# Performance work log

Measured on AMD Instinct MI355X. Metric: run time of the kernel, lower is better.

The kernel has to match this reference:

```python
import jax, jax.numpy as jnp
import numpy as np

SEQ_LEN = 12
EMB = 64        # embedding_dim
H = 128         # dec_h_dim
MLP = 1024      # mlp_dim
Z = 32          # z_dim
ZX = MLP + Z    # 1056, width of cat([enc_h_feat, z])
B = 32768


def setup_inputs() -> dict:
    key = jax.random.key(0)
    ks = jax.random.split(key, 16)
    s = 0.05  # weight scale to keep the recurrence stable
    return {
        "last_pos": jax.random.normal(ks[0], (B, 2), jnp.float32),
        "last_pos_rel": jax.random.normal(ks[1], (B, 2), jnp.float32),
        "enc_h_feat": jax.random.normal(ks[2], (B, MLP), jnp.float32),
        "z": jax.random.normal(ks[3], (B, Z), jnp.float32),
        "seq_start_end": jnp.zeros((1, 2), jnp.int64),
        # LSTM params (PyTorch layout: gates ordered i,f,g,o along rows)
        "W_ih": jax.random.normal(ks[4], (4 * H, ZX + EMB), jnp.float32) * s,
        "W_hh": jax.random.normal(ks[5], (4 * H, H), jnp.float32) * s,
        "b_ih": jax.random.normal(ks[6], (4 * H,), jnp.float32) * s,
        "b_hh": jax.random.normal(ks[7], (4 * H,), jnp.float32) * s,
        # mlp: Linear(ZX->MLP), ReLU, Linear(MLP->H), ReLU
        "W1": jax.random.normal(ks[8], (MLP, ZX), jnp.float32) * s,
        "b1": jax.random.normal(ks[9], (MLP,), jnp.float32) * s,
        "W2": jax.random.normal(ks[10], (H, MLP), jnp.float32) * s,
        "b2": jax.random.normal(ks[11], (H,), jnp.float32) * s,
        # spatial_embedding: Linear(2 -> EMB)
        "W_sp": jax.random.normal(ks[12], (EMB, 2), jnp.float32) * s,
        "b_sp": jax.random.normal(ks[13], (EMB,), jnp.float32) * s,
        # hidden2pos: Linear(H -> 2)
        "W_hp": jax.random.normal(ks[14], (2, H), jnp.float32) * s,
        "b_hp": jax.random.normal(ks[15], (2,), jnp.float32) * s,
    }


def _decode(last_pos, last_pos_rel, enc_h_feat, z,
            W_ih, W_hh, b_ih, b_hh, W1, b1, W2, b2, W_sp, b_sp, W_hp, b_hp):
    # initial decoder input from last relative position
    dec_inp = last_pos_rel @ W_sp.T + b_sp                     # [B, EMB]
    zx = jnp.concatenate([enc_h_feat, z], axis=1)              # [B, ZX]
    h = jax.nn.relu(jax.nn.relu(zx @ W1.T + b1) @ W2.T + b2)   # [B, H]
    c = jnp.zeros_like(h)
    # zx is constant across steps: precompute its gate contribution + biases
    W_zx, W_emb = W_ih[:, :ZX], W_ih[:, ZX:]
    zx_proj = zx @ W_zx.T + b_ih + b_hh                        # [B, 4H]

    def step(carry, _):
        h, c, last_pos, dec_inp = carry
        gates = zx_proj + dec_inp @ W_emb.T + h @ W_hh.T       # [B, 4H]
        i, f, g, o = jnp.split(gates, 4, axis=1)
        c = jax.nn.sigmoid(f) * c + jax.nn.sigmoid(i) * jnp.tanh(g)
        h = jax.nn.sigmoid(o) * jnp.tanh(c)
        rel_pos = h @ W_hp.T + b_hp                            # [B, 2]
        last_pos = rel_pos + last_pos
        dec_inp = rel_pos @ W_sp.T + b_sp
        return (h, c, last_pos, dec_inp), rel_pos

    _, pred = jax.lax.scan(step, (h, c, last_pos, dec_inp), None, length=SEQ_LEN)
    return pred  # [SEQ_LEN, B, 2]


def reference(last_pos, last_pos_rel, enc_h_feat, z, seq_start_end,
              W_ih, W_hh, b_ih, b_hh, W1, b1, W2, b2, W_sp, b_sp, W_hp, b_hp):
    # seq_start_end is unused by the original forward
    return _decode(last_pos, last_pos_rel, enc_h_feat, z,
                   W_ih, W_hh, b_ih, b_hh, W1, b1, W2, b2, W_sp, b_sp, W_hp, b_hp)
```

## Files before the change

### kernel.cpp

```cpp
#include <hip/hip_runtime.h>

#define BATCH   32768
#define SEQLEN  12
#define EMB     64
#define H       128
#define MLP     1024
#define Z       32
#define ZX      1056
#define KP      1088
#define NG      512

typedef _Float16 f16x8 __attribute__((ext_vector_type(8)));
typedef float    f32x4 __attribute__((ext_vector_type(4)));

#define S_WCAT_OFF   0u
#define S_W2H_OFF    3244032u
#define S_WHHF_OFF   3506176u
#define S_WC_OFF     3637248u
#define S_BIAS2_OFF  3641344u
#define S_T1_OFF     3643392u
#define S_GP_OFF     70752256u
#define S_H0_OFF     137861120u
#define B_WCAT_OFF   0u
#define B_W2H_OFF    3342336u
#define B_WHHF_OFF   3604480u
#define B_WC_OFF     3735552u
#define B_BIAS2_OFF  3739648u
#define B_T1_OFF     3741696u
#define B_GP_OFF     70850560u
#define B_H0_OFF     137959424u
#define B_ZX16_OFF   146348032u
#define B_TOTAL      217651200ull

__device__ __forceinline__ float sigf(float x) {
    return __builtin_amdgcn_rcpf(1.0f + __expf(-x));
}
__device__ __forceinline__ float tanhfast(float x) {
    return 2.0f * __builtin_amdgcn_rcpf(1.0f + __expf(-2.0f * x)) - 1.0f;
}

__device__ __forceinline__ void gload16(const void* g, void* l) {
    __builtin_amdgcn_global_load_lds(
        (const __attribute__((address_space(1))) unsigned int*)(unsigned long long)(uintptr_t)g,
        (__attribute__((address_space(3))) unsigned int*)(unsigned int)(uintptr_t)l,
        16, 0, 0);
}

__global__ __launch_bounds__(256) void prep_kernel(
    const float* __restrict__ W_ih, const float* __restrict__ W_hh_in,
    const float* __restrict__ b_ih, const float* __restrict__ b_hh,
    const float* __restrict__ W1,   const float* __restrict__ W2,
    const float* __restrict__ W_sp, const float* __restrict__ b_sp,
    const float* __restrict__ W_hp, int cs,
    _Float16* __restrict__ wcat, _Float16* __restrict__ w2h,
    _Float16* __restrict__ whhf, float* __restrict__ wc, float* __restrict__ bias2)
{
    const int bid = blockIdx.x;
    const int tid = threadIdx.x;
    if (bid < 1536) {
        const float* src = (bid < 1024) ? (W1 + (size_t)bid * ZX)
                                        : (W_ih + (size_t)(bid - 1024) * 1120);
        _Float16* dst = wcat + (size_t)bid * cs;
        for (int k = tid; k < cs; k += 256)
            dst[k] = (k < ZX) ? (_Float16)src[k] : (_Float16)0.f;
    } else if (bid < 1664) {
        const int n = bid - 1536;
        for (int k = tid; k < MLP; k += 256)
            w2h[n * MLP + k] = (_Float16)W2[n * MLP + k];
    } else if (bid < 1920) {
        const int n = (bid - 1664) * 2 + (tid >> 7);
        const int k = tid & 127;
        float wc0 = 0.f, wc1 = 0.f;
        for (int e = 0; e < EMB; ++e) {
            const float we = W_ih[(size_t)n * 1120 + ZX + e];
            wc0 += we * W_sp[e * 2];
            wc1 += we * W_sp[e * 2 + 1];
        }
        whhf[n * H + k] = (_Float16)(W_hh_in[n * H + k] + wc0 * W_hp[k] + wc1 * W_hp[H + k]);
    } else {
        const int t = (bid - 1920) * 256 + tid;
        if (t < 1024) {
            const int n = t >> 1, j = t & 1;
            float s = 0.f;
            for (int e = 0; e < EMB; ++e)
                s += W_ih[(size_t)n * 1120 + ZX + e] * W_sp[e * 2 + j];
            wc[t] = s;
        } else if (t < 1536) {
            const int n = t - 1024;
            float s = b_ih[n] + b_hh[n];
            for (int e = 0; e < EMB; ++e)
                s += W_ih[(size_t)n * 1120 + ZX + e] * b_sp[e];
            bias2[n] = s;
        }
    }
}

__global__ __launch_bounds__(256) void zxcast_kernel(
    const float* __restrict__ enc, const float* __restrict__ zin,
    _Float16* __restrict__ zx16)
{
    const int gid = blockIdx.x * 256 + threadIdx.x;
    if (gid < 4194304) {
        const int row = gid >> 7, cw = gid & 127;
        const float4* s = (const float4*)(enc + (size_t)row * MLP + cw * 8);
        const float4 f0 = s[0], f1 = s[1];
        f16x8 v = {(_Float16)f0.x, (_Float16)f0.y, (_Float16)f0.z, (_Float16)f0.w,
                   (_Float16)f1.x, (_Float16)f1.y, (_Float16)f1.z, (_Float16)f1.w};
        *(f16x8*)(zx16 + (size_t)row * KP + cw * 8) = v;
    } else if (gid < 4325376) {
        const int g2 = gid - 4194304;
        const int row = g2 >> 2, cw = g2 & 3;
        const float4* s = (const float4*)(zin + (size_t)row * Z + cw * 8);
        const float4 f0 = s[0], f1 = s[1];
        f16x8 v = {(_Float16)f0.x, (_Float16)f0.y, (_Float16)f0.z, (_Float16)f0.w,
                   (_Float16)f1.x, (_Float16)f1.y, (_Float16)f1.z, (_Float16)f1.w};
        *(f16x8*)(zx16 + (size_t)row * KP + MLP + cw * 8) = v;
    } else {
        const int g2 = gid - 4325376;
        const int row = g2 >> 2, cw = g2 & 3;
        f16x8 v = {};
        *(f16x8*)(zx16 + (size_t)row * KP + ZX + cw * 8) = v;
    }
}

__global__ __launch_bounds__(256) void gemm1_big_kernel(
    const _Float16* __restrict__ zx16, const _Float16* __restrict__ wcat,
    const float* __restrict__ bias1, const float* __restrict__ bias2g,
    _Float16* __restrict__ t1, float* __restrict__ gperm)
{
    __shared__ _Float16 s_a[128 * 64];
    __shared__ _Float16 s_b[128 * 64];

    const int tid = threadIdx.x;
    const int b = blockIdx.x;
    const int x = b & 7, s = b >> 3;
    const int mt = x * 32 + s / 12;
    const int bn = s % 12;
    const int m0 = mt * 128;

    const int lane = tid & 63, wv = tid >> 6;
    const int wm = wv >> 1, wn = wv & 1;
    const int l15 = lane & 15, q = lane >> 4;

    const int rowS = tid >> 3;
    const int chS  = (tid & 7) ^ ((tid >> 3) & 7);

    f32x4 acc[4][4] = {};

    for (int kt = 0; kt < 17; ++kt) {
        __syncthreads();
        #pragma unroll
        for (int i = 0; i < 4; ++i)
            gload16(zx16 + (size_t)(m0 + i * 32 + rowS) * KP + kt * 64 + chS * 8,
                    s_a + i * 2048 + wv * 512);
        #pragma unroll
        for (int i = 0; i < 4; ++i)
            gload16(wcat + (size_t)(bn * 128 + i * 32 + rowS) * KP + kt * 64 + chS * 8,
                    s_b + i * 2048 + wv * 512);
        __syncthreads();

        #pragma unroll
        for (int kt2 = 0; kt2 < 2; ++kt2) {
            f16x8 af[4];
            #pragma unroll
            for (int im = 0; im < 4; ++im) {
                const int row = wm * 64 + im * 16 + l15;
                const int ph  = (kt2 * 4 + q) ^ (l15 & 7);
                af[im] = *(const f16x8*)(s_a + row * 64 + ph * 8);
            }
            #pragma unroll
            for (int in_ = 0; in_ < 4; ++in_) {
                const int row = wn * 64 + in_ * 16 + l15;
                const int ph  = (kt2 * 4 + q) ^ (l15 & 7);
                const f16x8 bf = *(const f16x8*)(s_b + row * 64 + ph * 8);
                #pragma unroll
                for (int im = 0; im < 4; ++im)
                    acc[im][in_] = __builtin_amdgcn_mfma_f32_16x16x32_f16(af[im], bf, acc[im][in_], 0, 0, 0);
            }
        }
    }

    if (bn < 8) {
        #pragma unroll
        for (int im = 0; im < 4; ++im)
            #pragma unroll
            for (int in_ = 0; in_ < 4; ++in_) {
                const int n = bn * 128 + wn * 64 + in_ * 16 + l15;
                const float bb = bias1[n];
                #pragma unroll
                for (int r = 0; r < 4; ++r) {
                    const int m = m0 + wm * 64 + im * 16 + q * 4 + r;
                    float v = acc[im][in_][r] + bb;
                    v = v > 0.f ? v : 0.f;
                    t1[(size_t)m * MLP + n] = (_Float16)v;
                }
            }
    } else {
        #pragma unroll
        for (int im = 0; im < 4; ++im)
            #pragma unroll
            for (int in_ = 0; in_ < 4; ++in_) {
                const int n = (bn - 8) * 128 + wn * 64 + in_ * 16 + l15;
                const float bb = bias2g[n];
                const int m4 = (m0 + wm * 64 + im * 16 + q * 4) >> 2;
                float4 v;
                v.x = acc[im][in_][0] + bb;
                v.y = acc[im][in_][1] + bb;
                v.z = acc[im][in_][2] + bb;
                v.w = acc[im][in_][3] + bb;
                *(float4*)(gperm + ((size_t)m4 * NG + n) * 4) = v;
            }
    }
}

__global__ __launch_bounds__(256) void gemm1_small_kernel(
    const float* __restrict__ enc, const float* __restrict__ zin,
    const _Float16* __restrict__ wcat,
    const float* __restrict__ bias1, const float* __restrict__ bias2g,
    _Float16* __restrict__ t1, float* __restrict__ gperm)
{
    __shared__ float    s_a[128 * 32];
    __shared__ _Float16 s_b[128 * 32];

    const int tid = threadIdx.x;
    const int b = blockIdx.x;
    const int x = b & 7, s = b >> 3;
    const int mt = x * 32 + s / 12;
    const int bn = s % 12;
    const int m0 = mt * 128;

    const int lane = tid & 63, wv = tid >> 6;
    const int wm = wv >> 1, wn = wv & 1;
    const int l15 = lane & 15, q = lane >> 4;

    const int rowA = tid >> 3;
    const int chA  = (tid & 7) ^ ((tid >> 3) & 7);
    const int rowB = tid >> 2;
    const int chB  = (tid & 3) ^ ((tid >> 3) & 3);

    const int ca0 = (2 * q) ^ (l15 & 7);
    const int cb  = q ^ ((l15 >> 1) & 3);

    f32x4 acc[4][4] = {};

    for (int kt = 0; kt < 33; ++kt) {
        const float* abase;
        size_t astride;
        if (kt < 32) { abase = enc + (size_t)m0 * MLP + kt * 32; astride = MLP; }
        else         { abase = zin + (size_t)m0 * Z;             astride = Z;   }

        __syncthreads();
        #pragma unroll
        for (int i = 0; i < 4; ++i)
            gload16(abase + (size_t)(i * 32 + rowA) * astride + chA * 4,
                    s_a + i * 1024 + wv * 256);
        #pragma unroll
        for (int i = 0; i < 2; ++i)
            gload16(wcat + (size_t)(bn * 128 + i * 64 + rowB) * ZX + kt * 32 + chB * 8,
                    s_b + i * 2048 + wv * 512);
        __syncthreads();

        f16x8 af[4];
        #pragma unroll
        for (int im = 0; im < 4; ++im) {
            const float* ap = s_a + (wm * 64 + im * 16 + l15) * 32;
            const float4 f0 = *(const float4*)(ap + ca0 * 4);
            const float4 f1 = *(const float4*)(ap + (ca0 ^ 1) * 4);
            af[im] = f16x8{(_Float16)f0.x, (_Float16)f0.y, (_Float16)f0.z, (_Float16)f0.w,
                           (_Float16)f1.x, (_Float16)f1.y, (_Float16)f1.z, (_Float16)f1.w};
        }
        #pragma unroll
        for (int in_ = 0; in_ < 4; ++in_) {
            const f16x8 bf = *(const f16x8*)(s_b + (wn * 64 + in_ * 16 + l15) * 32 + cb * 8);
            #pragma unroll
            for (int im = 0; im < 4; ++im)
                acc[im][in_] = __builtin_amdgcn_mfma_f32_16x16x32_f16(af[im], bf, acc[im][in_], 0, 0, 0);
        }
    }

    if (bn < 8) {
        #pragma unroll
        for (int im = 0; im < 4; ++im)
            #pragma unroll
            for (int in_ = 0; in_ < 4; ++in_) {
                const int n = bn * 128 + wn * 64 + in_ * 16 + l15;
                const float bb = bias1[n];
                #pragma unroll
                for (int r = 0; r < 4; ++r) {
                    const int m = m0 + wm * 64 + im * 16 + q * 4 + r;
                    float v = acc[im][in_][r] + bb;
                    v = v > 0.f ? v : 0.f;
                    t1[(size_t)m * MLP + n] = (_Float16)v;
                }
            }
    } else {
        #pragma unroll
        for (int im = 0; im < 4; ++im)
            #pragma unroll
            for (int in_ = 0; in_ < 4; ++in_) {
                const int n = (bn - 8) * 128 + wn * 64 + in_ * 16 + l15;
                const float bb = bias2g[n];
                const int m4 = (m0 + wm * 64 + im * 16 + q * 4) >> 2;
                float4 v;
                v.x = acc[im][in_][0] + bb;
                v.y = acc[im][in_][1] + bb;
                v.z = acc[im][in_][2] + bb;
                v.w = acc[im][in_][3] + bb;
                *(float4*)(gperm + ((size_t)m4 * NG + n) * 4) = v;
            }
    }
}

__global__ __launch_bounds__(256) void gemm2_kernel(
    const _Float16* __restrict__ t1, const _Float16* __restrict__ w2h,
    const float* __restrict__ b2, _Float16* __restrict__ h0buf)
{
    __shared__ _Float16 s_a[64 * 32];
    __shared__ _Float16 s_b[128 * 32];

    const int tid = threadIdx.x;
    const int m0  = blockIdx.x * 64;
    const int lane = tid & 63, wv = tid >> 6;
    const int l15 = lane & 15, q = lane >> 4;

    const int rowS = tid >> 2;
    const int chS  = ((tid & 3) ^ (tid >> 2) ^ (tid >> 4)) & 3;
    const int phF  = (q ^ l15 ^ (l15 >> 2)) & 3;

    f32x4 acc[4][2] = {};

    for (int kt = 0; kt < 32; ++kt) {
        __syncthreads();
        gload16(t1 + (size_t)(m0 + rowS) * MLP + kt * 32 + chS * 8,
                s_a + wv * 512);
        #pragma unroll
        for (int i = 0; i < 2; ++i) {
            const int row = i * 64 + rowS;
            const int c   = ((tid & 3) ^ row ^ (row >> 2)) & 3;
            gload16(w2h + (size_t)row * MLP + kt * 32 + c * 8,
                    s_b + i * 2048 + wv * 512);
        }
        __syncthreads();

        f16x8 af[4];
        #pragma unroll
        for (int im = 0; im < 4; ++im)
            af[im] = *(const f16x8*)(s_a + (im * 16 + l15) * 32 + phF * 8);
        #pragma unroll
        for (int in_ = 0; in_ < 2; ++in_) {
            const f16x8 bf = *(const f16x8*)(s_b + (wv * 32 + in_ * 16 + l15) * 32 + phF * 8);
            #pragma unroll
            for (int im = 0; im < 4; ++im)
                acc[im][in_] = __builtin_amdgcn_mfma_f32_16x16x32_f16(af[im], bf, acc[im][in_], 0, 0, 0);
        }
    }

    #pragma unroll
    for (int im = 0; im < 4; ++im)
        #pragma unroll
        for (int in_ = 0; in_ < 2; ++in_) {
            const int n = wv * 32 + in_ * 16 + l15;
            const float bb = b2[n];
            #pragma unroll
            for (int r = 0; r < 4; ++r) {
                const int m = m0 + im * 16 + q * 4 + r;
                float v = acc[im][in_][r] + bb;
                v = v > 0.f ? v : 0.f;
                h0buf[(size_t)m * H + n] = (_Float16)v;
            }
        }
}

__global__ __launch_bounds__(512) void recur_kernel(
    const float* __restrict__ gperm, const _Float16* __restrict__ h0buf,
    const _Float16* __restrict__ whhf, const float* __restrict__ wc,
    const float* __restrict__ whp, const float* __restrict__ bhp,
    const float* __restrict__ lpr, float* __restrict__ out)
{
    __shared__ _Float16 s_whh[512 * 136];
    __shared__ _Float16 s_h[64 * 136];
    __shared__ float    s_p[128];
    __shared__ float    s_wc[1024];
    __shared__ float    s_whp[256];
    __shared__ float    s_bhp[2];

    const int tid = threadIdx.x;
    const int m0  = blockIdx.x * 64;
    const int lane = tid & 63, w = tid >> 6;
    const int l15 = lane & 15, q = lane >> 4;

    #pragma unroll
    for (int i = 0; i < 16; ++i) {
        const int cid = tid + i * 512;
        const int row = cid >> 4, ch = cid & 15;
        *(uint4*)(s_whh + row * 136 + ch * 8) = *(const uint4*)(whhf + row * H + ch * 8);
    }
    if (tid < 256) *(float4*)(s_wc + tid * 4)  = *(const float4*)(wc + tid * 4);
    if (tid < 64)  *(float4*)(s_whp + tid * 4) = *(const float4*)(whp + tid * 4);
    if (tid < 2)   s_bhp[tid] = bhp[tid];
    if (tid < 128) s_p[tid] = lpr[(size_t)m0 * 2 + tid];
    {
        const int row = tid >> 3, ch = tid & 7;
        *(uint4*)(s_h + row * 136 + ch * 16)     = *(const uint4*)(h0buf + (size_t)(m0 + row) * H + ch * 16);
        *(uint4*)(s_h + row * 136 + ch * 16 + 8) = *(const uint4*)(h0buf + (size_t)(m0 + row) * H + ch * 16 + 8);
    }

    f32x4 gb[4][4];
    #pragma unroll
    for (int im = 0; im < 4; ++im) {
        const int m4 = (m0 >> 2) + im * 4 + q;
        #pragma unroll
        for (int g = 0; g < 4; ++g) {
            const float4 v = *(const float4*)(gperm + ((size_t)m4 * NG + g * H + w * 16 + l15) * 4);
            gb[im][g] = f32x4{v.x, v.y, v.z, v.w};
        }
    }

    f32x4 cst[4] = {};

    __syncthreads();

    {
        const int part = tid & 3;
        const int j    = (tid >> 2) & 1;
        const int row  = tid >> 3;
        float sum = 0.f;
        #pragma unroll
        for (int u = 0; u < 4; ++u) {
            const f16x8 hv = *(const f16x8*)(s_h + row * 136 + part * 32 + u * 8);
            const float4* wp = (const float4*)(s_whp + j * H + part * 32 + u * 8);
            const float4 w0 = wp[0], w1 = wp[1];
            sum += (float)hv[0] * w0.x + (float)hv[1] * w0.y + (float)hv[2] * w0.z + (float)hv[3] * w0.w
                 + (float)hv[4] * w1.x + (float)hv[5] * w1.y + (float)hv[6] * w1.z + (float)hv[7] * w1.w;
        }
        sum += __shfl_down(sum, 2, 64);
        sum += __shfl_down(sum, 1, 64);
        if (part == 0) s_p[row * 2 + j] -= sum;
    }
    __syncthreads();

    float wc0[4], wc1[4], cg[4];
    #pragma unroll
    for (int g = 0; g < 4; ++g) {
        const int n = g * H + w * 16 + l15;
        wc0[g] = s_wc[n * 2];
        wc1[g] = s_wc[n * 2 + 1];
        cg[g]  = wc0[g] * s_bhp[0] + wc1[g] * s_bhp[1];
    }
    #pragma unroll
    for (int im = 0; im < 4; ++im)
        #pragma unroll
        for (int r = 0; r < 4; ++r) {
            const int mrow = im * 16 + q * 4 + r;
            const float pa = s_p[mrow * 2], pb = s_p[mrow * 2 + 1];
            #pragma unroll
            for (int g = 0; g < 4; ++g)
                gb[im][g][r] += pa * wc0[g] + pb * wc1[g];
        }

    for (int t = 0; t < SEQLEN; ++t) {
        f32x4 acc[4][4];
        #pragma unroll
        for (int kt = 0; kt < 4; ++kt) {
            f16x8 af[4];
            #pragma unroll
            for (int im = 0; im < 4; ++im)
                af[im] = *(const f16x8*)(s_h + (im * 16 + l15) * 136 + kt * 32 + q * 8);
            #pragma unroll
            for (int g = 0; g < 4; ++g) {
                const f16x8 bf = *(const f16x8*)(s_whh + (g * H + w * 16 + l15) * 136 + kt * 32 + q * 8);
                #pragma unroll
                for (int im = 0; im < 4; ++im)
                    acc[im][g] = __builtin_amdgcn_mfma_f32_16x16x32_f16(
                        af[im], bf, (kt == 0) ? gb[im][g] : acc[im][g], 0, 0, 0);
            }
        }
        __syncthreads();

        #pragma unroll
        for (int im = 0; im < 4; ++im) {
            #pragma unroll
            for (int r = 0; r < 4; ++r) {
                const int mrow = im * 16 + q * 4 + r;
                const float cc = sigf(acc[im][1][r]) * cst[im][r]
                               + sigf(acc[im][0][r]) * tanhfast(acc[im][2][r]);
                cst[im][r] = cc;
                const float hh = sigf(acc[im][3][r]) * tanhfast(cc);
                s_h[mrow * 136 + w * 16 + l15] = (_Float16)hh;
            }
        }
        if (t == 0) {
            #pragma unroll
            for (int im = 0; im < 4; ++im)
                #pragma unroll
                for (int r = 0; r < 4; ++r) {
                    const int mrow = im * 16 + q * 4 + r;
                    const float pa = s_p[mrow * 2], pb = s_p[mrow * 2 + 1];
                    #pragma unroll
                    for (int g = 0; g < 4; ++g)
                        gb[im][g][r] += cg[g] - (pa * wc0[g] + pb * wc1[g]);
                }
        }
        __syncthreads();

        {
            const int part = tid & 3;
            const int j    = (tid >> 2) & 1;
            const int row  = tid >> 3;
            float sum = 0.f;
            #pragma unroll
            for (int u = 0; u < 4; ++u) {
                const f16x8 hv = *(const f16x8*)(s_h + row * 136 + part * 32 + u * 8);
                const float4* wp = (const float4*)(s_whp + j * H + part * 32 + u * 8);
                const float4 w0 = wp[0], w1 = wp[1];
                sum += (float)hv[0] * w0.x + (float)hv[1] * w0.y + (float)hv[2] * w0.z + (float)hv[3] * w0.w
                     + (float)hv[4] * w1.x + (float)hv[5] * w1.y + (float)hv[6] * w1.z + (float)hv[7] * w1.w;
            }
            sum += __shfl_down(sum, 2, 64);
            sum += __shfl_down(sum, 1, 64);
            if (part == 0)
                out[(size_t)t * (BATCH * 2) + (size_t)(m0 + row) * 2 + j] = sum + s_bhp[j];
        }
    }
}

extern "C" void kernel_launch(void* const* d_in, const int* in_sizes, int n_in,
                              void* d_out, int out_size, void* d_ws, size_t ws_size,
                              hipStream_t stream)
{
    const float* last_pos_rel = (const float*)d_in[1];
    const float* enc          = (const float*)d_in[2];
    const float* zin          = (const float*)d_in[3];
    const float* W_ih         = (const float*)d_in[5];
    const float* W_hh         = (const float*)d_in[6];
    const float* b_ih         = (const float*)d_in[7];
    const float* b_hh         = (const float*)d_in[8];
    const float* W1           = (const float*)d_in[9];
    const float* b1           = (const float*)d_in[10];
    const float* W2           = (const float*)d_in[11];
    const float* b2           = (const float*)d_in[12];
    const float* W_sp         = (const float*)d_in[13];
    const float* b_sp         = (const float*)d_in[14];
    const float* W_hp         = (const float*)d_in[15];
    const float* b_hp         = (const float*)d_in[16];
    float* out = (float*)d_out;

    char* ws = (char*)d_ws;
    const bool big = (ws_size >= B_TOTAL);

    _Float16* wcat  = (_Float16*)(ws + (big ? B_WCAT_OFF  : S_WCAT_OFF));
    _Float16* w2h   = (_Float16*)(ws + (big ? B_W2H_OFF   : S_W2H_OFF));
    _Float16* whhf  = (_Float16*)(ws + (big ? B_WHHF_OFF  : S_WHHF_OFF));
    float*    wc    = (float*)(ws + (big ? B_WC_OFF    : S_WC_OFF));
    float*    bias2 = (float*)(ws + (big ? B_BIAS2_OFF : S_BIAS2_OFF));
    _Float16* t1    = (_Float16*)(ws + (big ? B_T1_OFF : S_T1_OFF));
    float*    gperm = (float*)(ws + (big ? B_GP_OFF : S_GP_OFF));
    _Float16* h0b   = (_Float16*)(ws + (big ? B_H0_OFF : S_H0_OFF));
    _Float16* zx16  = (_Float16*)(ws + B_ZX16_OFF);

    prep_kernel<<<dim3(1926), 256, 0, stream>>>(W_ih, W_hh, b_ih, b_hh, W1, W2, W_sp, b_sp,
                                                W_hp, big ? KP : ZX, wcat, w2h, whhf, wc, bias2);
    if (big) {
        zxcast_kernel<<<dim3(17408), 256, 0, stream>>>(enc, zin, zx16);
        gemm1_big_kernel<<<dim3(3072), 256, 0, stream>>>(zx16, wcat, b1, bias2, t1, gperm);
    } else {
        gemm1_small_kernel<<<dim3(3072), 256, 0, stream>>>(enc, zin, wcat, b1, bias2, t1, gperm);
    }
    gemm2_kernel<<<dim3(512), 256, 0, stream>>>(t1, w2h, b2, h0b);
    recur_kernel<<<dim3(512), 512, 0, stream>>>(gperm, h0b, whhf, wc, W_hp, b_hp,
                                                last_pos_rel, out);
}
```

Baseline: 532.1 us.

## Double-buffer 256x256 GEMM1 tiles with interleaved async loads and MFMA priority

Restructures the big first GEMM to use 256x256 output tiles per 512-thread block with double-buffered LDS. Global-to-LDS loads for the next K slice are split into quarters and issued between MFMA phases, using explicit waitcnt/barrier and s_setprio to overlap memory with compute. The larger tile cuts redundant global traffic per FLOP and the launch drops to 768 blocks. In exchange it uses 128 KB of shared memory per block and 128 accumulator registers per thread, which may limit occupancy and risks pressure or spills.

Result: faster. 482.7 us (-9.3%).

```diff
diff --git a/kernel.cpp b/kernel.cpp
--- a/kernel.cpp
+++ b/kernel.cpp
@@ -123,86 +123,186 @@
     }
 }
 
-__global__ __launch_bounds__(256) void gemm1_big_kernel(
+__global__ __launch_bounds__(512, 2) void gemm1_big_kernel(
     const _Float16* __restrict__ zx16, const _Float16* __restrict__ wcat,
     const float* __restrict__ bias1, const float* __restrict__ bias2g,
     _Float16* __restrict__ t1, float* __restrict__ gperm)
 {
-    __shared__ _Float16 s_a[128 * 64];
-    __shared__ _Float16 s_b[128 * 64];
+    __shared__ _Float16 s_a[2][256 * 64];
+    __shared__ _Float16 s_b[2][256 * 64];
 
     const int tid = threadIdx.x;
-    const int b = blockIdx.x;
-    const int x = b & 7, s = b >> 3;
-    const int mt = x * 32 + s / 12;
-    const int bn = s % 12;
-    const int m0 = mt * 128;
+    const int b   = blockIdx.x;
+    const int swz = (b & 7) * 96 + (b >> 3);
+    const int mt  = swz / 6, nt = swz % 6;
+    const int m0  = mt * 256, n0 = nt * 256;
 
     const int lane = tid & 63, wv = tid >> 6;
-    const int wm = wv >> 1, wn = wv & 1;
-    const int l15 = lane & 15, q = lane >> 4;
+    const int wm   = wv >> 2,  wn = wv & 3;
+    const int l15  = lane & 15, q = lane >> 4;
 
     const int rowS = tid >> 3;
-    const int chS  = (tid & 7) ^ ((tid >> 3) & 7);
-
-    f32x4 acc[4][4] = {};
-
-    for (int kt = 0; kt < 17; ++kt) {
-        __syncthreads();
-        #pragma unroll
-        for (int i = 0; i < 4; ++i)
-            gload16(zx16 + (size_t)(m0 + i * 32 + rowS) * KP + kt * 64 + chS * 8,
-                    s_a + i * 2048 + wv * 512);
-        #pragma unroll
-        for (int i = 0; i < 4; ++i)
-            gload16(wcat + (size_t)(bn * 128 + i * 32 + rowS) * KP + kt * 64 + chS * 8,
-                    s_b + i * 2048 + wv * 512);
-        __syncthreads();
-
-        #pragma unroll
-        for (int kt2 = 0; kt2 < 2; ++kt2) {
-            f16x8 af[4];
-            #pragma unroll
-            for (int im = 0; im < 4; ++im) {
-                const int row = wm * 64 + im * 16 + l15;
-                const int ph  = (kt2 * 4 + q) ^ (l15 & 7);
-                af[im] = *(const f16x8*)(s_a + row * 64 + ph * 8);
-            }
+    const int chS  = (tid & 7) ^ (rowS & 7);
+
+    const _Float16* gA = zx16 + (size_t)(m0 + rowS) * KP + chS * 8;
+    const _Float16* gB = wcat + (size_t)(n0 + rowS) * KP + chS * 8;
+    const size_t rstep = (size_t)64 * KP;
+
+    const int ph0  = q ^ (l15 & 7);
+    const int ph1  = (4 + q) ^ (l15 & 7);
+    const int aof0 = (wm * 128 + l15) * 64 + ph0 * 8;
+    const int aof1 = (wm * 128 + l15) * 64 + ph1 * 8;
+    const int bof0 = (wn * 64 + l15) * 64 + ph0 * 8;
+    const int bof1 = (wn * 64 + l15) * 64 + ph1 * 8;
+
+    f32x4 acc[8][4] = {};
+
+    {
+        _Float16* dA = &s_a[0][0] + wv * 512;
+        _Float16* dB = &s_b[0][0] + wv * 512;
+        #pragma unroll
+        for (int j = 0; j < 4; ++j) gload16(gA + j * rstep, dA + j * 4096);
+        #pragma unroll
+        for (int j = 0; j < 4; ++j) gload16(gB + j * rstep, dB + j * 4096);
+    }
+
+    #pragma unroll 2
+    for (int kt = 0; kt < 16; ++kt) {
+        const int cur = kt & 1;
+        const _Float16* sA = &s_a[cur][0];
+        const _Float16* sB = &s_b[cur][0];
+        _Float16* dA = &s_a[cur ^ 1][0] + wv * 512;
+        _Float16* dB = &s_b[cur ^ 1][0] + wv * 512;
+        const _Float16* gA1 = gA + (kt + 1) * 64;
+        const _Float16* gB1 = gB + (kt + 1) * 64;
+
+        f16x8 af[4], bf[4];
+
+        gload16(gA1,         dA);
+        gload16(gA1 + rstep, dA + 4096);
+        asm volatile("s_waitcnt vmcnt(2)\n\ts_barrier" ::: "memory");
+        #pragma unroll
+        for (int i = 0; i < 4; ++i) af[i] = *(const f16x8*)(sA + aof0 + i * 1024);
+        #pragma unroll
+        for (int i = 0; i < 4; ++i) bf[i] = *(const f16x8*)(sB + bof0 + i * 1024);
+        __builtin_amdgcn_s_setprio(1);
+        #pragma unroll
+        for (int n_ = 0; n_ < 4; ++n_)
+            #pragma unroll
+            for (int m_ = 0; m_ < 4; ++m_)
+                acc[m_][n_] = __builtin_amdgcn_mfma_f32_16x16x32_f16(af[m_], bf[n_], acc[m_][n_], 0, 0, 0);
+        __builtin_amdgcn_s_setprio(0);
+        asm volatile("s_barrier" ::: "memory");
+
+        gload16(gA1 + 2 * rstep, dA + 8192);
+        gload16(gA1 + 3 * rstep, dA + 12288);
+        #pragma unroll
+        for (int i = 0; i < 4; ++i) af[i] = *(const f16x8*)(sA + aof0 + 4096 + i * 1024);
+        asm volatile("s_barrier" ::: "memory");
+        __builtin_amdgcn_s_setprio(1);
+        #pragma unroll
+        for (int n_ = 0; n_ < 4; ++n_)
+            #pragma unroll
+            for (int m_ = 0; m_ < 4; ++m_)
+                acc[4 + m_][n_] = __builtin_amdgcn_mfma_f32_16x16x32_f16(af[m_], bf[n_], acc[4 + m_][n_], 0, 0, 0);
+        __builtin_amdgcn_s_setprio(0);
+        asm volatile("s_barrier" ::: "memory");
+
+        gload16(gB1,         dB);
+        gload16(gB1 + rstep, dB + 4096);
+        #pragma unroll
+        for (int i = 0; i < 4; ++i) af[i] = *(const f16x8*)(sA + aof1 + i * 1024);
+        #pragma unroll
+        for (int i = 0; i < 4; ++i) bf[i] = *(const f16x8*)(sB + bof1 + i * 1024);
+        asm volatile("s_barrier" ::: "memory");
+        __builtin_amdgcn_s_setprio(1);
+        #pragma unroll
+        for (int n_ = 0; n_ < 4; ++n_)
+            #pragma unroll
+            for (int m_ = 0; m_ < 4; ++m_)
+                acc[m_][n_] = __builtin_amdgcn_mfma_f32_16x16x32_f16(af[m_], bf[n_], acc[m_][n_], 0, 0, 0);
+        __builtin_amdgcn_s_setprio(0);
+        asm volatile("s_barrier" ::: "memory");
+
+        gload16(gB1 + 2 * rstep, dB + 8192);
+        gload16(gB1 + 3 * rstep, dB + 12288);
+        #pragma unroll
+        for (int i = 0; i < 4; ++i) af[i] = *(const f16x8*)(sA + aof1 + 4096 + i * 1024);
+        asm volatile("s_barrier" ::: "memory");
+        __builtin_amdgcn_s_setprio(1);
+        #pragma unroll
+        for (int n_ = 0; n_ < 4; ++n_)
+            #pragma unroll
+            for (int m_ = 0; m_ < 4; ++m_)
+                acc[4 + m_][n_] = __builtin_amdgcn_mfma_f32_16x16x32_f16(af[m_], bf[n_], acc[4 + m_][n_], 0, 0, 0);
+        __builtin_amdgcn_s_setprio(0);
+        asm volatile("s_barrier" ::: "memory");
+    }
+
+    {
+        const _Float16* sA = &s_a[0][0];
+        const _Float16* sB = &s_b[0][0];
+        asm volatile("s_waitcnt vmcnt(0)\n\ts_barrier" ::: "memory");
+        f16x8 af[4], bf[4];
+        #pragma unroll
+        for (int i = 0; i < 4; ++i) af[i] = *(const f16x8*)(sA + aof0 + i * 1024);
+        #pragma unroll
+        for (int i = 0; i < 4; ++i) bf[i] = *(const f16x8*)(sB + bof0 + i * 1024);
+        __builtin_amdgcn_s_setprio(1);
+        #pragma unroll
+        for (int n_ = 0; n_ < 4; ++n_)
+            #pragma unroll
+            for (int m_ = 0; m_ < 4; ++m_)
+                acc[m_][n_] = __builtin_amdgcn_mfma_f32_16x16x32_f16(af[m_], bf[n_], acc[m_][n_], 0, 0, 0);
+        #pragma unroll
+        for (int i = 0; i < 4; ++i) af[i] = *(const f16x8*)(sA + aof0 + 4096 + i * 1024);
+        #pragma unroll
+        for (int n_ = 0; n_ < 4; ++n_)
+            #pragma unroll
+            for (int m_ = 0; m_ < 4; ++m_)
+                acc[4 + m_][n_] = __builtin_amdgcn_mfma_f32_16x16x32_f16(af[m_], bf[n_], acc[4 + m_][n_], 0, 0, 0);
+        #pragma unroll
+        for (int i = 0; i < 4; ++i) af[i] = *(const f16x8*)(sA + aof1 + i * 1024);
+        #pragma unroll
+        for (int i = 0; i < 4; ++i) bf[i] = *(const f16x8*)(sB + bof1 + i * 1024);
+        #pragma unroll
+        for (int n_ = 0; n_ < 4; ++n_)
+            #pragma unroll
+            for (int m_ = 0; m_ < 4; ++m_)
+                acc[m_][n_] = __builtin_amdgcn_mfma_f32_16x16x32_f16(af[m_], bf[n_], acc[m_][n_], 0, 0, 0);
+        #pragma unroll
+        for (int i = 0; i < 4; ++i) af[i] = *(const f16x8*)(sA + aof1 + 4096 + i * 1024);
+        #pragma unroll
+        for (int n_ = 0; n_ < 4; ++n_)
+            #pragma unroll
+            for (int m_ = 0; m_ < 4; ++m_)
+                acc[4 + m_][n_] = __builtin_amdgcn_mfma_f32_16x16x32_f16(af[m_], bf[n_], acc[4 + m_][n_], 0, 0, 0);
+        __builtin_amdgcn_s_setprio(0);
+    }
+
+    if (nt < 4) {
+        #pragma unroll
+        for (int im = 0; im < 8; ++im)
             #pragma unroll
             for (int in_ = 0; in_ < 4; ++in_) {
-                const int row = wn * 64 + in_ * 16 + l15;
-                const int ph  = (kt2 * 4 + q) ^ (l15 & 7);
-                const f16x8 bf = *(const f16x8*)(s_b + row * 64 + ph * 8);
-                #pragma unroll
-                for (int im = 0; im < 4; ++im)
-                    acc[im][in_] = __builtin_amdgcn_mfma_f32_16x16x32_f16(af[im], bf, acc[im][in_], 0, 0, 0);
-            }
-        }
-    }
-
-    if (bn < 8) {
-        #pragma unroll
-        for (int im = 0; im < 4; ++im)
-            #pragma unroll
-            for (int in_ = 0; in_ < 4; ++in_) {
-                const int n = bn * 128 + wn * 64 + in_ * 16 + l15;
+                const int n = n0 + wn * 64 + in_ * 16 + l15;
                 const float bb = bias1[n];
+                const int mbase = m0 + wm * 128 + im * 16 + q * 4;
                 #pragma unroll
                 for (int r = 0; r < 4; ++r) {
-                    const int m = m0 + wm * 64 + im * 16 + q * 4 + r;
                     float v = acc[im][in_][r] + bb;
                     v = v > 0.f ? v : 0.f;
-                    t1[(size_t)m * MLP + n] = (_Float16)v;
+                    t1[(size_t)(mbase + r) * MLP + n] = (_Float16)v;
                 }
             }
     } else {
         #pragma unroll
-        for (int im = 0; im < 4; ++im)
+        for (int im = 0; im < 8; ++im)
             #pragma unroll
             for (int in_ = 0; in_ < 4; ++in_) {
-                const int n = (bn - 8) * 128 + wn * 64 + in_ * 16 + l15;
+                const int n = (n0 - 1024) + wn * 64 + in_ * 16 + l15;
                 const float bb = bias2g[n];
-                const int m4 = (m0 + wm * 64 + im * 16 + q * 4) >> 2;
+                const int m4 = (m0 + wm * 128 + im * 16 + q * 4) >> 2;
                 float4 v;
                 v.x = acc[im][in_][0] + bb;
                 v.y = acc[im][in_][1] + bb;
@@ -562,7 +662,7 @@
                                                 W_hp, big ? KP : ZX, wcat, w2h, whhf, wc, bias2);
     if (big) {
         zxcast_kernel<<<dim3(17408), 256, 0, stream>>>(enc, zin, zx16);
-        gemm1_big_kernel<<<dim3(3072), 256, 0, stream>>>(zx16, wcat, b1, bias2, t1, gperm);
+        gemm1_big_kernel<<<dim3(768), 512, 0, stream>>>(zx16, wcat, b1, bias2, t1, gperm);
     } else {
         gemm1_small_kernel<<<dim3(3072), 256, 0, stream>>>(enc, zin, wcat, b1, bias2, t1, gperm);
     }
```
